# Kernel tuning notes

Measured on AMD Instinct MI355X. Metric: run time of the kernel, lower is better.

## Reference

```python
import jax, jax.numpy as jnp
import numpy as np

WH, WW = 8, 8          # window size
NH = 8                 # num heads
ED = 256               # embed dim
HD = ED // NH          # head dim
SCALE = HD ** -0.5


def setup_inputs() -> dict:
    key = jax.random.key(0)
    k1, k2, k3, k4 = jax.random.split(key, 4)
    x = jax.random.normal(k1, (8, ED, 128, 128), dtype=jnp.float32)
    w_qkv = jax.random.normal(k2, (3 * ED, ED), dtype=jnp.float32) * (ED ** -0.5)
    w_out = jax.random.normal(k3, (ED, ED), dtype=jnp.float32) * (ED ** -0.5)
    b_out = jax.random.normal(k4, (ED,), dtype=jnp.float32) * 0.01
    return {"x": x, "w_qkv": w_qkv, "w_out": w_out, "b_out": b_out}


def reference(x, w_qkv, w_out, b_out):
    # x: [B, C, H, W] (NCHW) -> [B, H, W, C]
    x = jnp.transpose(x, (0, 2, 3, 1))
    B, H, W, C = x.shape
    pad_h = (WH - H % WH) % WH
    pad_w = (WW - W % WW) % WW
    x = jnp.pad(x, ((0, 0), (0, pad_h), (0, pad_w), (0, 0)))
    Hp, Wp = H + pad_h, W + pad_w
    nh, nw = Hp // WH, Wp // WW
    N = WH * WW
    # window partition -> [B*nh*nw, N, C]
    xw = x.reshape(B, nh, WH, nw, WW, C).transpose(0, 1, 3, 2, 4, 5).reshape(-1, N, C)
    # qkv projection (no bias): [nW, N, 3, NH, HD]
    qkv = (xw @ w_qkv.T).reshape(-1, N, 3, NH, HD)
    q, k, v = qkv[:, :, 0], qkv[:, :, 1], qkv[:, :, 2]  # [nW, N, NH, HD]
    # NOTE: faithful to source — attention across the HEADS axis per token
    attn = jnp.einsum('wnhd,wngd->wnhg', q, k) * SCALE  # [nW, N, NH, NH]
    attn = jax.nn.softmax(attn, axis=-1)
    out = jnp.einsum('wnhg,wngd->wnhd', attn, v)        # [nW, N, NH, HD]
    # torch: transpose(1,2).reshape(-1, N, C)
    out = out.transpose(0, 2, 1, 3).reshape(-1, N, C)
    out = out @ w_out.T + b_out
    # window merge
    out = out.reshape(B, nh, nw, WH, WW, C).transpose(0, 1, 3, 2, 4, 5).reshape(B, Hp, Wp, C)
    out = out[:, :H, :W, :]
    # faithful final permute(0,3,2,1): [B, C, W, H]
    return jnp.transpose(out, (0, 3, 2, 1))
```

## Files before the change

### kernel.cpp

```cpp
#include <hip/hip_runtime.h>

#define SCALE 0.17677669529663687f

typedef __attribute__((ext_vector_type(8))) short bf16x8;
typedef __attribute__((ext_vector_type(4))) float f32x4;

__device__ __forceinline__ unsigned short f2bf(float f) {
    unsigned u = __float_as_uint(f);
    u += 0x7FFFu + ((u >> 16) & 1u);
    return (unsigned short)(u >> 16);
}
__device__ __forceinline__ float bf2f(unsigned short s) {
    return __uint_as_float(((unsigned)s) << 16);
}
__device__ __forceinline__ unsigned pk2c(float a, float b) {
    return (unsigned)f2bf(a) | ((unsigned)f2bf(b) << 16);
}

__global__ __launch_bounds__(256) void wconv_kernel(
        const float* __restrict__ w_qkv, const float* __restrict__ w_out,
        unsigned short* __restrict__ wq, unsigned short* __restrict__ wo) {
    int idx = blockIdx.x * 256 + threadIdx.x;
    if (idx < 196608) wq[idx] = f2bf(w_qkv[idx]);
    else if (idx < 262144) wo[idx - 196608] = f2bf(w_out[idx - 196608]);
}

__global__ __launch_bounds__(512, 4) void qkv_attn_fused_kernel(
        const float* __restrict__ x, const unsigned short* __restrict__ wq,
        unsigned short* __restrict__ o_ws) {
    __shared__ unsigned char lds[65536];
    const int tid = threadIdx.x;
    const int tb  = blockIdx.x << 5;
    const int b   = tb >> 14;
    const float* xb = x + (size_t)b * 4194304 + (tb & 16383);

    {
        const int tok   = tid & 31;
        const int cbase = (tid >> 5) * 16;
        float f[16];
        #pragma unroll
        for (int e = 0; e < 16; ++e)
            f[e] = xb[(size_t)(cbase + e) * 16384 + tok];
        #pragma unroll
        for (int hlf = 0; hlf < 2; ++hlf) {
            const int c0 = cbase + hlf * 8;
            unsigned u0 = pk2c(f[hlf*8+0], f[hlf*8+1]), u1 = pk2c(f[hlf*8+2], f[hlf*8+3]);
            unsigned u2 = pk2c(f[hlf*8+4], f[hlf*8+5]), u3 = pk2c(f[hlf*8+6], f[hlf*8+7]);
            const int slot = (c0 >> 3) ^ (tok & 7);
            *(uint4*)(lds + tok * 512 + (slot << 4)) = make_uint4(u0, u1, u2, u3);
        }
    }
    __syncthreads();

    const int lane = tid & 63;
    const int wave = tid >> 6;
    const int lrow = lane & 15, lk = lane >> 4;
    const int j0w = wave * 96;

    f32x4 acc[2][6];
    #pragma unroll
    for (int mt = 0; mt < 2; ++mt)
        #pragma unroll
        for (int nt = 0; nt < 6; ++nt)
            acc[mt][nt] = (f32x4){0.f, 0.f, 0.f, 0.f};
    #pragma unroll
    for (int k = 0; k < 8; ++k) {
        bf16x8 a[2], bb[6];
        #pragma unroll
        for (int mt = 0; mt < 2; ++mt) {
            int t = mt * 16 + lrow;
            int slot = (k * 4 + lk) ^ (t & 7);
            a[mt] = *(const bf16x8*)(lds + t * 512 + (slot << 4));
        }
        #pragma unroll
        for (int nt = 0; nt < 6; ++nt) {
            int j = j0w + nt * 16 + lrow;
            bb[nt] = *(const bf16x8*)((const unsigned char*)wq + (size_t)j * 512 + k * 64 + lk * 16);
        }
        #pragma unroll
        for (int mt = 0; mt < 2; ++mt)
            #pragma unroll
            for (int nt = 0; nt < 6; ++nt)
                acc[mt][nt] = __builtin_amdgcn_mfma_f32_16x16x32_bf16(a[mt], bb[nt], acc[mt][nt], 0, 0, 0);
    }
    #pragma unroll
    for (int mt = 0; mt < 2; ++mt)
        #pragma unroll
        for (int nt = 0; nt < 6; ++nt)
            #pragma unroll
            for (int i = 0; i < 4; ++i) {
                int t = mt * 16 + lk * 4 + i;
                int ch = j0w + nt * 16 + lrow;
                int slot = (ch >> 3) ^ (t & 7);
                *(unsigned short*)(lds + 16384 + t * 1536 + (slot << 4) + (ch & 7) * 2) = f2bf(acc[mt][nt][i]);
            }
    __syncthreads();

    {
        const int t  = tid >> 4;
        const int h  = (tid >> 1) & 7;
        const int hf = tid & 1;
        const int tx = t & 7;
        const unsigned char* row = lds + 16384 + t * 1536;
        float q[16];
        #pragma unroll
        for (int jj = 0; jj < 2; ++jj) {
            int slot = (h * 4 + hf * 2 + jj) ^ tx;
            bf16x8 v = *(const bf16x8*)(row + (slot << 4));
            #pragma unroll
            for (int e = 0; e < 8; ++e) q[jj * 8 + e] = bf2f((unsigned short)v[e]);
        }
        float dots[8];
        #pragma unroll
        for (int g = 0; g < 8; ++g) {
            float acc2 = 0.f;
            #pragma unroll
            for (int jj = 0; jj < 2; ++jj) {
                int slot = (32 + g * 4 + hf * 2 + jj) ^ tx;
                bf16x8 v = *(const bf16x8*)(row + (slot << 4));
                #pragma unroll
                for (int e = 0; e < 8; ++e) acc2 += q[jj * 8 + e] * bf2f((unsigned short)v[e]);
            }
            dots[g] = acc2;
        }
        #pragma unroll
        for (int g = 0; g < 8; ++g)
            dots[g] = (dots[g] + __shfl_xor(dots[g], 1, 64)) * SCALE;
        float mx = dots[0];
        #pragma unroll
        for (int g = 1; g < 8; ++g) mx = fmaxf(mx, dots[g]);
        float sum = 0.f;
        #pragma unroll
        for (int g = 0; g < 8; ++g) { dots[g] = __expf(dots[g] - mx); sum += dots[g]; }
        const float inv = 1.f / sum;
        float o[16];
        #pragma unroll
        for (int d = 0; d < 16; ++d) o[d] = 0.f;
        #pragma unroll
        for (int g = 0; g < 8; ++g) {
            const float p = dots[g] * inv;
            #pragma unroll
            for (int jj = 0; jj < 2; ++jj) {
                int slot = (64 + g * 4 + hf * 2 + jj) ^ tx;
                bf16x8 v = *(const bf16x8*)(row + (slot << 4));
                #pragma unroll
                for (int e = 0; e < 8; ++e) o[jj * 8 + e] += p * bf2f((unsigned short)v[e]);
            }
        }
        const int tok = tb + t;
        const int bb2 = tok >> 14, rem = tok & 16383;
        const int himg = rem >> 7, wimg = rem & 127;
        const int ih = himg >> 3, r = himg & 7;
        const int iw = wimg >> 3, s = wimg & 7;
        const int win = (bb2 << 8) + (ih << 4) + iw;
        unsigned short* dst = o_ws + ((size_t)win * 64 + h * 8 + r) * 256 + s * 32 + hf * 16;
        #pragma unroll
        for (int jj = 0; jj < 2; ++jj) {
            uint4 v = make_uint4(pk2c(o[jj * 8 + 0], o[jj * 8 + 1]), pk2c(o[jj * 8 + 2], o[jj * 8 + 3]),
                                 pk2c(o[jj * 8 + 4], o[jj * 8 + 5]), pk2c(o[jj * 8 + 6], o[jj * 8 + 7]));
            *(uint4*)(dst + jj * 8) = v;
        }
    }
}

__global__ __launch_bounds__(512, 6) void outproj_kernel(
        const unsigned short* __restrict__ o_ws, const unsigned short* __restrict__ wo,
        const float* __restrict__ b_out, float* __restrict__ out) {
    __shared__ unsigned char lds[32768];
    const int tid = threadIdx.x;
    const int bid = blockIdx.x;
    const int b  = bid >> 8;
    const int ih = (bid >> 4) & 15;
    const int iw = bid & 15;

    {
        const unsigned char* src = (const unsigned char*)(o_ws + (size_t)bid * 16384);
        #pragma unroll
        for (int it = 0; it < 4; ++it) {
            int q = it * 512 + tid;
            int np = q >> 5;
            int slot = (q & 31) ^ (np & 7);
            *(bf16x8*)(lds + np * 512 + (slot << 4)) = *(const bf16x8*)(src + q * 16);
        }
    }
    __syncthreads();

    const int lane = tid & 63;
    const int wave = tid >> 6;
    const int lrow = lane & 15;
    const int lk   = lane >> 4;
    const int j0 = wave * 32;

    f32x4 acc[4][2];
    #pragma unroll
    for (int mt = 0; mt < 4; ++mt)
        #pragma unroll
        for (int nt = 0; nt < 2; ++nt)
            acc[mt][nt] = (f32x4){0.f, 0.f, 0.f, 0.f};
    #pragma unroll
    for (int k = 0; k < 8; ++k) {
        bf16x8 a[4], bb[2];
        #pragma unroll
        for (int mt = 0; mt < 4; ++mt) {
            int t = mt * 16 + lrow;
            int slot = (k * 4 + lk) ^ (t & 7);
            a[mt] = *(const bf16x8*)(lds + t * 512 + (slot << 4));
        }
        #pragma unroll
        for (int nt = 0; nt < 2; ++nt) {
            int j = j0 + nt * 16 + lrow;
            bb[nt] = *(const bf16x8*)((const unsigned char*)wo + (size_t)j * 512 + k * 64 + lk * 16);
        }
        #pragma unroll
        for (int mt = 0; mt < 4; ++mt)
            #pragma unroll
            for (int nt = 0; nt < 2; ++nt)
                acc[mt][nt] = __builtin_amdgcn_mfma_f32_16x16x32_bf16(a[mt], bb[nt], acc[mt][nt], 0, 0, 0);
    }
    float bias[2];
    #pragma unroll
    for (int nt = 0; nt < 2; ++nt) bias[nt] = b_out[j0 + nt * 16 + lrow];
    __syncthreads();

    const size_t obase = ((size_t)b * 256) * 16384 + (size_t)(iw * 8) * 128 + ih * 8;
    #pragma unroll
    for (int half = 0; half < 2; ++half) {
        if ((wave >> 2) == half) {
            int jl = (wave & 3) * 32;
            #pragma unroll
            for (int mt = 0; mt < 4; ++mt)
                #pragma unroll
                for (int nt = 0; nt < 2; ++nt)
                    #pragma unroll
                    for (int i = 0; i < 4; ++i) {
                        int t = mt * 16 + lk * 4 + i;
                        int el = jl + nt * 16 + lrow;
                        int sl = (el >> 2) ^ (t & 7);
                        *(float*)(lds + t * 512 + (sl << 4) + (el & 3) * 4) = acc[mt][nt][i] + bias[nt];
                    }
        }
        __syncthreads();
        #pragma unroll
        for (int it = 0; it < 2; ++it) {
            int idx = it * 512 + tid;
            int el = idx >> 3, sp = idx & 7;
            float vals[8];
            #pragma unroll
            for (int rp = 0; rp < 8; ++rp) {
                int t = rp * 8 + sp;
                int sl = (el >> 2) ^ (t & 7);
                vals[rp] = *(const float*)(lds + t * 512 + (sl << 4) + (el & 3) * 4);
            }
            float* po = out + obase + (size_t)(half * 128 + el) * 16384 + sp * 128;
            *(float4*)po       = make_float4(vals[0], vals[1], vals[2], vals[3]);
            *(float4*)(po + 4) = make_float4(vals[4], vals[5], vals[6], vals[7]);
        }
        __syncthreads();
    }
}

extern "C" void kernel_launch(void* const* d_in, const int* in_sizes, int n_in,
                              void* d_out, int out_size, void* d_ws, size_t ws_size,
                              hipStream_t stream) {
    const float* x     = (const float*)d_in[0];
    const float* w_qkv = (const float*)d_in[1];
    const float* w_out = (const float*)d_in[2];
    const float* b_out = (const float*)d_in[3];
    float* out = (float*)d_out;

    const size_t O_BYTES = 67108864;

    unsigned short* o_ws = (unsigned short*)d_ws;
    unsigned short* wq   = (unsigned short*)((char*)d_ws + O_BYTES);
    unsigned short* wo   = wq + 196608;

    wconv_kernel<<<dim3(1024), dim3(256), 0, stream>>>(w_qkv, w_out, wq, wo);
    qkv_attn_fused_kernel<<<dim3(4096), dim3(512), 0, stream>>>(x, wq, o_ws);
    outproj_kernel<<<dim3(2048), dim3(512), 0, stream>>>(o_ws, wo, b_out, out);
}
```

Before: 282.8 us.

## Compute per-token head attention with MFMA and stage output through LDS

```diff
diff --git a/kernel.cpp b/kernel.cpp
--- a/kernel.cpp
+++ b/kernel.cpp
@@ -86,79 +86,99 @@
     #pragma unroll
     for (int mt = 0; mt < 2; ++mt)
         #pragma unroll
-        for (int nt = 0; nt < 6; ++nt)
+        for (int nt = 0; nt < 6; ++nt) {
+            const int chg = j0w + nt * 16;
             #pragma unroll
             for (int i = 0; i < 4; ++i) {
-                int t = mt * 16 + lk * 4 + i;
-                int ch = j0w + nt * 16 + lrow;
-                int slot = (ch >> 3) ^ (t & 7);
-                *(unsigned short*)(lds + 16384 + t * 1536 + (slot << 4) + (ch & 7) * 2) = f2bf(acc[mt][nt][i]);
-            }
+                const int t = mt * 16 + lk * 4 + i;
+                const int ch = chg + lrow;
+                unsigned short v = f2bf(acc[mt][nt][i]);
+                if (chg < 512) {
+                    int c = ch >> 3, slot = c ^ (t & 7);
+                    *(unsigned short*)(lds + 16384 + t * 1536 + (slot << 4) + (ch & 7) * 2) = v;
+                } else {
+                    int g = (ch - 512) >> 5, d = (ch - 512) & 31;
+                    *(unsigned short*)(lds + 16384 + t * 1536 + 1024 + d * 16 + g * 2) = v;
+                }
+            }
+        }
     __syncthreads();
 
     {
-        const int t  = tid >> 4;
-        const int h  = (tid >> 1) & 7;
-        const int hf = tid & 1;
-        const int tx = t & 7;
-        const unsigned char* row = lds + 16384 + t * 1536;
-        float q[16];
-        #pragma unroll
-        for (int jj = 0; jj < 2; ++jj) {
-            int slot = (h * 4 + hf * 2 + jj) ^ tx;
-            bf16x8 v = *(const bf16x8*)(row + (slot << 4));
-            #pragma unroll
-            for (int e = 0; e < 8; ++e) q[jj * 8 + e] = bf2f((unsigned short)v[e]);
-        }
-        float dots[8];
-        #pragma unroll
-        for (int g = 0; g < 8; ++g) {
-            float acc2 = 0.f;
-            #pragma unroll
-            for (int jj = 0; jj < 2; ++jj) {
-                int slot = (32 + g * 4 + hf * 2 + jj) ^ tx;
-                bf16x8 v = *(const bf16x8*)(row + (slot << 4));
-                #pragma unroll
-                for (int e = 0; e < 8; ++e) acc2 += q[jj * 8 + e] * bf2f((unsigned short)v[e]);
-            }
-            dots[g] = acc2;
-        }
-        #pragma unroll
-        for (int g = 0; g < 8; ++g)
-            dots[g] = (dots[g] + __shfl_xor(dots[g], 1, 64)) * SCALE;
-        float mx = dots[0];
-        #pragma unroll
-        for (int g = 1; g < 8; ++g) mx = fmaxf(mx, dots[g]);
-        float sum = 0.f;
-        #pragma unroll
-        for (int g = 0; g < 8; ++g) { dots[g] = __expf(dots[g] - mx); sum += dots[g]; }
-        const float inv = 1.f / sum;
-        float o[16];
-        #pragma unroll
-        for (int d = 0; d < 16; ++d) o[d] = 0.f;
-        #pragma unroll
-        for (int g = 0; g < 8; ++g) {
-            const float p = dots[g] * inv;
-            #pragma unroll
-            for (int jj = 0; jj < 2; ++jj) {
-                int slot = (64 + g * 4 + hf * 2 + jj) ^ tx;
-                bf16x8 v = *(const bf16x8*)(row + (slot << 4));
-                #pragma unroll
-                for (int e = 0; e < 8; ++e) o[jj * 8 + e] += p * bf2f((unsigned short)v[e]);
-            }
-        }
-        const int tok = tb + t;
-        const int bb2 = tok >> 14, rem = tok & 16383;
-        const int himg = rem >> 7, wimg = rem & 127;
+        const int col   = lane & 15;
+        const int chunk = lane >> 4;
+        unsigned char* Pbuf = lds + wave * 1280;
+        const int tcol = (col >> 3);
+        const int g    = col & 7;
+        const int tloc = (chunk >> 1);
+        const bool valid = (tloc == tcol);
+
+        #pragma unroll
+        for (int p = 0; p < 2; ++p) {
+            const int T0 = wave * 4 + p * 2;
+            bf16x8 qf, kf;
+            {
+                const int trow = T0 + (col >> 3);
+                const int hh = col & 7;
+                const int cq = hh * 4 + chunk;
+                qf = *(const bf16x8*)(lds + 16384 + trow * 1536 + (((cq) ^ (trow & 7)) << 4));
+                const int ck = 32 + hh * 4 + chunk;
+                kf = *(const bf16x8*)(lds + 16384 + trow * 1536 + (((ck) ^ (trow & 7)) << 4));
+            }
+            f32x4 s = __builtin_amdgcn_mfma_f32_16x16x32_bf16(qf, kf, (f32x4){0.f,0.f,0.f,0.f}, 0, 0, 0);
+            float pvls[4];
+            #pragma unroll
+            for (int i = 0; i < 4; ++i) {
+                float si = s[i] * SCALE;
+                float m = si;
+                m = fmaxf(m, __shfl_xor(m, 1, 64));
+                m = fmaxf(m, __shfl_xor(m, 2, 64));
+                m = fmaxf(m, __shfl_xor(m, 4, 64));
+                float e = __expf(si - m);
+                float su = e;
+                su += __shfl_xor(su, 1, 64);
+                su += __shfl_xor(su, 2, 64);
+                su += __shfl_xor(su, 4, 64);
+                pvls[i] = e / su;
+            }
+            #pragma unroll
+            for (int i = 0; i < 4; ++i) {
+                const int r = chunk * 4 + i;
+                unsigned short pb = valid ? f2bf(pvls[i]) : (unsigned short)0;
+                *(unsigned short*)(Pbuf + r * 80 + tcol * 32 + g * 2) = pb;
+                *(unsigned short*)(Pbuf + r * 80 + tcol * 32 + 16 + g * 2) = 0;
+            }
+            bf16x8 pf = *(const bf16x8*)(Pbuf + col * 80 + chunk * 16);
+            const int tv = T0 + (chunk >> 1);
+            bf16x8 vf0 = *(const bf16x8*)(lds + 16384 + tv * 1536 + 1024 + (col << 4));
+            bf16x8 vf1 = *(const bf16x8*)(lds + 16384 + tv * 1536 + 1024 + ((16 + col) << 4));
+            f32x4 o0 = __builtin_amdgcn_mfma_f32_16x16x32_bf16(pf, vf0, (f32x4){0.f,0.f,0.f,0.f}, 0, 0, 0);
+            f32x4 o1 = __builtin_amdgcn_mfma_f32_16x16x32_bf16(pf, vf1, (f32x4){0.f,0.f,0.f,0.f}, 0, 0, 0);
+            #pragma unroll
+            for (int i = 0; i < 4; ++i) {
+                const int ro = chunk * 4 + i;
+                const int tO = T0 + (ro >> 3);
+                const int hO = ro & 7;
+                *(unsigned short*)(lds + 16384 + tO * 1536 + hO * 64 + col * 2)        = f2bf(o0[i]);
+                *(unsigned short*)(lds + 16384 + tO * 1536 + hO * 64 + (16 + col) * 2) = f2bf(o1[i]);
+            }
+        }
+    }
+    __syncthreads();
+
+    {
+        const int himg = (tb & 16383) >> 7;
         const int ih = himg >> 3, r = himg & 7;
-        const int iw = wimg >> 3, s = wimg & 7;
-        const int win = (bb2 << 8) + (ih << 4) + iw;
-        unsigned short* dst = o_ws + ((size_t)win * 64 + h * 8 + r) * 256 + s * 32 + hf * 16;
-        #pragma unroll
-        for (int jj = 0; jj < 2; ++jj) {
-            uint4 v = make_uint4(pk2c(o[jj * 8 + 0], o[jj * 8 + 1]), pk2c(o[jj * 8 + 2], o[jj * 8 + 3]),
-                                 pk2c(o[jj * 8 + 4], o[jj * 8 + 5]), pk2c(o[jj * 8 + 6], o[jj * 8 + 7]));
-            *(uint4*)(dst + jj * 8) = v;
+        const int win0 = (b << 8) + (ih << 4) + ((tb & 127) >> 3);
+        #pragma unroll
+        for (int it = 0; it < 2; ++it) {
+            const int q = it * 512 + tid;
+            const int dchunk = q & 3;
+            const int sloc   = (q >> 2) & 7;
+            const int h      = (q >> 5) & 7;
+            const int wloc   = q >> 8;
+            bf16x8 v = *(const bf16x8*)(lds + 16384 + (size_t)(wloc * 8 + sloc) * 1536 + h * 64 + dchunk * 16);
+            *(bf16x8*)(o_ws + (size_t)(win0 + wloc) * 16384 + (h * 8 + r) * 256 + sloc * 32 + dchunk * 8) = v;
         }
     }
 }
```

Result: slower. 288.8 us (+2.1%).

## Double-buffer QKV weight loads, raise MFMA priority, pack bf16 pair stores

Applied to the files above, without the earlier changes.

```diff
diff --git a/kernel.cpp b/kernel.cpp
--- a/kernel.cpp
+++ b/kernel.cpp
@@ -63,37 +63,75 @@
         #pragma unroll
         for (int nt = 0; nt < 6; ++nt)
             acc[mt][nt] = (f32x4){0.f, 0.f, 0.f, 0.f};
-    #pragma unroll
-    for (int k = 0; k < 8; ++k) {
-        bf16x8 a[2], bb[6];
-        #pragma unroll
-        for (int mt = 0; mt < 2; ++mt) {
-            int t = mt * 16 + lrow;
-            int slot = (k * 4 + lk) ^ (t & 7);
-            a[mt] = *(const bf16x8*)(lds + t * 512 + (slot << 4));
-        }
+    {
+        const unsigned char* wqb = (const unsigned char*)wq;
+        bf16x8 b0[6], b1[6];
         #pragma unroll
         for (int nt = 0; nt < 6; ++nt) {
-            int j = j0w + nt * 16 + lrow;
-            bb[nt] = *(const bf16x8*)((const unsigned char*)wq + (size_t)j * 512 + k * 64 + lk * 16);
-        }
-        #pragma unroll
-        for (int mt = 0; mt < 2; ++mt)
-            #pragma unroll
-            for (int nt = 0; nt < 6; ++nt)
-                acc[mt][nt] = __builtin_amdgcn_mfma_f32_16x16x32_bf16(a[mt], bb[nt], acc[mt][nt], 0, 0, 0);
+            int j = j0w + (nt >> 1) * 32 + lrow * 2 + (nt & 1);
+            b0[nt] = *(const bf16x8*)(wqb + (size_t)j * 512 + 0 * 64 + lk * 16);
+        }
+        #pragma unroll
+        for (int k = 0; k < 8; k += 2) {
+            #pragma unroll
+            for (int nt = 0; nt < 6; ++nt) {
+                int j = j0w + (nt >> 1) * 32 + lrow * 2 + (nt & 1);
+                b1[nt] = *(const bf16x8*)(wqb + (size_t)j * 512 + (k + 1) * 64 + lk * 16);
+            }
+            {
+                bf16x8 a[2];
+                #pragma unroll
+                for (int mt = 0; mt < 2; ++mt) {
+                    int t = mt * 16 + lrow;
+                    int slot = (k * 4 + lk) ^ (t & 7);
+                    a[mt] = *(const bf16x8*)(lds + t * 512 + (slot << 4));
+                }
+                __builtin_amdgcn_s_setprio(1);
+                #pragma unroll
+                for (int mt = 0; mt < 2; ++mt)
+                    #pragma unroll
+                    for (int nt = 0; nt < 6; ++nt)
+                        acc[mt][nt] = __builtin_amdgcn_mfma_f32_16x16x32_bf16(a[mt], b0[nt], acc[mt][nt], 0, 0, 0);
+                __builtin_amdgcn_s_setprio(0);
+            }
+            if (k + 2 < 8) {
+                #pragma unroll
+                for (int nt = 0; nt < 6; ++nt) {
+                    int j = j0w + (nt >> 1) * 32 + lrow * 2 + (nt & 1);
+                    b0[nt] = *(const bf16x8*)(wqb + (size_t)j * 512 + (k + 2) * 64 + lk * 16);
+                }
+            }
+            {
+                bf16x8 a[2];
+                #pragma unroll
+                for (int mt = 0; mt < 2; ++mt) {
+                    int t = mt * 16 + lrow;
+                    int slot = ((k + 1) * 4 + lk) ^ (t & 7);
+                    a[mt] = *(const bf16x8*)(lds + t * 512 + (slot << 4));
+                }
+                __builtin_amdgcn_s_setprio(1);
+                #pragma unroll
+                for (int mt = 0; mt < 2; ++mt)
+                    #pragma unroll
+                    for (int nt = 0; nt < 6; ++nt)
+                        acc[mt][nt] = __builtin_amdgcn_mfma_f32_16x16x32_bf16(a[mt], b1[nt], acc[mt][nt], 0, 0, 0);
+                __builtin_amdgcn_s_setprio(0);
+            }
+        }
     }
     #pragma unroll
     for (int mt = 0; mt < 2; ++mt)
         #pragma unroll
-        for (int nt = 0; nt < 6; ++nt)
+        for (int pr = 0; pr < 3; ++pr) {
+            const int ch0 = j0w + pr * 32 + lrow * 2;
             #pragma unroll
             for (int i = 0; i < 4; ++i) {
-                int t = mt * 16 + lk * 4 + i;
-                int ch = j0w + nt * 16 + lrow;
-                int slot = (ch >> 3) ^ (t & 7);
-                *(unsigned short*)(lds + 16384 + t * 1536 + (slot << 4) + (ch & 7) * 2) = f2bf(acc[mt][nt][i]);
-            }
+                const int t = mt * 16 + lk * 4 + i;
+                const int slot = (ch0 >> 3) ^ (t & 7);
+                unsigned pv = pk2c(acc[mt][2 * pr][i], acc[mt][2 * pr + 1][i]);
+                *(unsigned*)(lds + 16384 + t * 1536 + (slot << 4) + (ch0 & 7) * 2) = pv;
+            }
+        }
     __syncthreads();
 
     {
```

Result: no change. 287.4 us (+1.6%).

## Process 64 tokens per block in fused QKV-attention kernel with larger LDS

Applied to the files above, without the earlier changes.

```diff
diff --git a/kernel.cpp b/kernel.cpp
--- a/kernel.cpp
+++ b/kernel.cpp
@@ -23,6 +23,144 @@
     int idx = blockIdx.x * 256 + threadIdx.x;
     if (idx < 196608) wq[idx] = f2bf(w_qkv[idx]);
     else if (idx < 262144) wo[idx - 196608] = f2bf(w_out[idx - 196608]);
+}
+
+__global__ __launch_bounds__(1024, 4) void qkv_attn_fused64_kernel(
+        const float* __restrict__ x, const unsigned short* __restrict__ wq,
+        unsigned short* __restrict__ o_ws) {
+    extern __shared__ unsigned char lds[];
+    const int tid = threadIdx.x;
+    const int tb  = blockIdx.x << 6;
+    const int b   = tb >> 14;
+    const float* xb = x + (size_t)b * 4194304 + (tb & 16383);
+
+    {
+        const int tok   = tid & 63;
+        const int cbase = (tid >> 6) * 16;
+        float f[16];
+        #pragma unroll
+        for (int e = 0; e < 16; ++e)
+            f[e] = xb[(size_t)(cbase + e) * 16384 + tok];
+        #pragma unroll
+        for (int hlf = 0; hlf < 2; ++hlf) {
+            const int c0 = cbase + hlf * 8;
+            unsigned u0 = pk2c(f[hlf*8+0], f[hlf*8+1]), u1 = pk2c(f[hlf*8+2], f[hlf*8+3]);
+            unsigned u2 = pk2c(f[hlf*8+4], f[hlf*8+5]), u3 = pk2c(f[hlf*8+6], f[hlf*8+7]);
+            const int slot = (c0 >> 3) ^ (tok & 7);
+            *(uint4*)(lds + tok * 512 + (slot << 4)) = make_uint4(u0, u1, u2, u3);
+        }
+    }
+    __syncthreads();
+
+    const int lane = tid & 63;
+    const int wave = tid >> 6;
+    const int lrow = lane & 15, lk = lane >> 4;
+    const int j0w = wave * 48;
+
+    f32x4 acc[4][3];
+    #pragma unroll
+    for (int mt = 0; mt < 4; ++mt)
+        #pragma unroll
+        for (int nt = 0; nt < 3; ++nt)
+            acc[mt][nt] = (f32x4){0.f, 0.f, 0.f, 0.f};
+    #pragma unroll
+    for (int k = 0; k < 8; ++k) {
+        bf16x8 a[4], bb[3];
+        #pragma unroll
+        for (int mt = 0; mt < 4; ++mt) {
+            int t = mt * 16 + lrow;
+            int slot = (k * 4 + lk) ^ (t & 7);
+            a[mt] = *(const bf16x8*)(lds + t * 512 + (slot << 4));
+        }
+        #pragma unroll
+        for (int nt = 0; nt < 3; ++nt) {
+            int j = j0w + nt * 16 + lrow;
+            bb[nt] = *(const bf16x8*)((const unsigned char*)wq + (size_t)j * 512 + k * 64 + lk * 16);
+        }
+        #pragma unroll
+        for (int mt = 0; mt < 4; ++mt)
+            #pragma unroll
+            for (int nt = 0; nt < 3; ++nt)
+                acc[mt][nt] = __builtin_amdgcn_mfma_f32_16x16x32_bf16(a[mt], bb[nt], acc[mt][nt], 0, 0, 0);
+    }
+    #pragma unroll
+    for (int mt = 0; mt < 4; ++mt)
+        #pragma unroll
+        for (int nt = 0; nt < 3; ++nt)
+            #pragma unroll
+            for (int i = 0; i < 4; ++i) {
+                int t = mt * 16 + lk * 4 + i;
+                int ch = j0w + nt * 16 + lrow;
+                int slot = (ch >> 3) ^ (t & 7);
+                *(unsigned short*)(lds + 32768 + t * 1536 + (slot << 4) + (ch & 7) * 2) = f2bf(acc[mt][nt][i]);
+            }
+    __syncthreads();
+
+    {
+        const int t  = tid >> 4;
+        const int h  = (tid >> 1) & 7;
+        const int hf = tid & 1;
+        const int tx = t & 7;
+        const unsigned char* row = lds + 32768 + t * 1536;
+        float q[16];
+        #pragma unroll
+        for (int jj = 0; jj < 2; ++jj) {
+            int slot = (h * 4 + hf * 2 + jj) ^ tx;
+            bf16x8 v = *(const bf16x8*)(row + (slot << 4));
+            #pragma unroll
+            for (int e = 0; e < 8; ++e) q[jj * 8 + e] = bf2f((unsigned short)v[e]);
+        }
+        float dots[8];
+        #pragma unroll
+        for (int g = 0; g < 8; ++g) {
+            float acc2 = 0.f;
+            #pragma unroll
+            for (int jj = 0; jj < 2; ++jj) {
+                int slot = (32 + g * 4 + hf * 2 + jj) ^ tx;
+                bf16x8 v = *(const bf16x8*)(row + (slot << 4));
+                #pragma unroll
+                for (int e = 0; e < 8; ++e) acc2 += q[jj * 8 + e] * bf2f((unsigned short)v[e]);
+            }
+            dots[g] = acc2;
+        }
+        #pragma unroll
+        for (int g = 0; g < 8; ++g)
+            dots[g] = (dots[g] + __shfl_xor(dots[g], 1, 64)) * SCALE;
+        float mx = dots[0];
+        #pragma unroll
+        for (int g = 1; g < 8; ++g) mx = fmaxf(mx, dots[g]);
+        float sum = 0.f;
+        #pragma unroll
+        for (int g = 0; g < 8; ++g) { dots[g] = __expf(dots[g] - mx); sum += dots[g]; }
+        const float inv = 1.f / sum;
+        float o[16];
+        #pragma unroll
+        for (int d = 0; d < 16; ++d) o[d] = 0.f;
+        #pragma unroll
+        for (int g = 0; g < 8; ++g) {
+            const float p = dots[g] * inv;
+            #pragma unroll
+            for (int jj = 0; jj < 2; ++jj) {
+                int slot = (64 + g * 4 + hf * 2 + jj) ^ tx;
+                bf16x8 v = *(const bf16x8*)(row + (slot << 4));
+                #pragma unroll
+                for (int e = 0; e < 8; ++e) o[jj * 8 + e] += p * bf2f((unsigned short)v[e]);
+            }
+        }
+        const int tok = tb + t;
+        const int bb2 = tok >> 14, rem = tok & 16383;
+        const int himg = rem >> 7, wimg = rem & 127;
+        const int ih = himg >> 3, r = himg & 7;
+        const int iw = wimg >> 3, s = wimg & 7;
+        const int win = (bb2 << 8) + (ih << 4) + iw;
+        unsigned short* dst = o_ws + ((size_t)win * 64 + h * 8 + r) * 256 + s * 32 + hf * 16;
+        #pragma unroll
+        for (int jj = 0; jj < 2; ++jj) {
+            uint4 v = make_uint4(pk2c(o[jj * 8 + 0], o[jj * 8 + 1]), pk2c(o[jj * 8 + 2], o[jj * 8 + 3]),
+                                 pk2c(o[jj * 8 + 4], o[jj * 8 + 5]), pk2c(o[jj * 8 + 6], o[jj * 8 + 7]));
+            *(uint4*)(dst + jj * 8) = v;
+        }
+    }
 }
 
 __global__ __launch_bounds__(512, 4) void qkv_attn_fused_kernel(
@@ -275,6 +413,15 @@
     unsigned short* wo   = wq + 196608;
 
     wconv_kernel<<<dim3(1024), dim3(256), 0, stream>>>(w_qkv, w_out, wq, wo);
-    qkv_attn_fused_kernel<<<dim3(4096), dim3(512), 0, stream>>>(x, wq, o_ws);
+
+    hipError_t aerr = hipFuncSetAttribute(
+        reinterpret_cast<const void*>(qkv_attn_fused64_kernel),
+        hipFuncAttributeMaxDynamicSharedMemorySize, 131072);
+    if (aerr == hipSuccess) {
+        qkv_attn_fused64_kernel<<<dim3(2048), dim3(1024), 131072, stream>>>(x, wq, o_ws);
+    } else {
+        qkv_attn_fused_kernel<<<dim3(4096), dim3(512), 0, stream>>>(x, wq, o_ws);
+    }
+
     outproj_kernel<<<dim3(2048), dim3(512), 0, stream>>>(o_ws, wo, b_out, out);
 }
```

Measured after the change: 235.2 us (median of 2 runs). 16.8% less time.
